# Performance work log

Measured on AMD Instinct MI355X. Metric: run time of the kernel, lower is better.

The kernel has to match this reference:

```python
import jax, jax.numpy as jnp
import numpy as np

E = 8            # num_experts
H = 1024         # hidden_size
I = 1024         # moe_intermediate_dim
T = 8192         # total tokens (sum of per-expert counts; no padding, grouped_mm path)
# Imbalanced routing, sums exactly to T
COUNTS = np.array([512, 1536, 1024, 768, 1280, 896, 1152, 1024], dtype=np.int32)


def setup_inputs() -> dict:
    key = jax.random.key(0)
    k_x, k_gu, k_d = jax.random.split(key, 3)
    x = jax.random.normal(k_x, (T, H), dtype=jnp.float32)
    # Weights stored pre-transposed: (E, H, 2I) and (E, I, H)
    gate_up_proj = jax.random.normal(k_gu, (E, H, 2 * I), dtype=jnp.float32) * (1.0 / np.sqrt(H))
    down_proj = jax.random.normal(k_d, (E, I, H), dtype=jnp.float32) * (1.0 / np.sqrt(I))
    num_tokens_per_expert = jnp.asarray(COUNTS)  # int32, sums to T
    return {
        "x": x,
        "gate_up_proj": gate_up_proj,
        "down_proj": down_proj,
        "num_tokens_per_expert": num_tokens_per_expert,
    }


def reference(x, gate_up_proj, down_proj, num_tokens_per_expert):
    # Grouped GEMM 1: [T,H] x [E,H,2I] with ragged group sizes -> [T,2I]
    gate_up = jax.lax.ragged_dot(x, gate_up_proj, group_sizes=num_tokens_per_expert)
    gate, up = jnp.split(gate_up, 2, axis=-1)
    h = jax.nn.silu(gate) * up  # SwiGLU: silu(gate) * up, [T,I]
    # Grouped GEMM 2: [T,I] x [E,I,H] -> [T,H]
    out = jax.lax.ragged_dot(h, down_proj, group_sizes=num_tokens_per_expert)
    return out.astype(x.dtype)
```

## Files before the change

### kernel.cpp

```cpp
#include <hip/hip_runtime.h>
#include <hip/hip_bf16.h>
#include <stdint.h>

#define E_ 8
#define H_ 1024
#define I_ 1024
#define T_ 8192
#define BM 128
#define BK 32
#define NKT 32

typedef __attribute__((ext_vector_type(4))) float f32x4;
typedef __attribute__((ext_vector_type(8))) short bf16x8;

__device__ __forceinline__ unsigned short f2bf(float f) {
  union { float f; unsigned int u; } v; v.f = f;
  unsigned int lsb = (v.u >> 16) & 1u;
  v.u += 0x7fffu + lsb;
  return (unsigned short)(v.u >> 16);
}

__device__ __forceinline__ void gload_lds16(const void* g, void* l) {
  __builtin_amdgcn_global_load_lds(
      (const __attribute__((address_space(1))) unsigned int*)g,
      (__attribute__((address_space(3))) unsigned int*)l,
      16, 0, 0);
}

__global__ void convert_f32_bf16(const float* __restrict__ in,
                                 unsigned short* __restrict__ out, int n) {
  int i = (blockIdx.x * blockDim.x + threadIdx.x) * 4;
  if (i >= n) return;
  float4 v = *reinterpret_cast<const float4*>(in + i);
  ushort4 o;
  o.x = f2bf(v.x); o.y = f2bf(v.y); o.z = f2bf(v.z); o.w = f2bf(v.w);
  *reinterpret_cast<ushort4*>(out + i) = o;
}

__global__ void transpose_f32_to_bf16(const float* __restrict__ in,
                                      unsigned short* __restrict__ out,
                                      int R, int C) {
  __shared__ float tile[64][33];
  int e = blockIdx.z;
  const float* inp = in + (size_t)e * R * C;
  unsigned short* outp = out + (size_t)e * R * C;
  int c0 = blockIdx.x * 32, r0 = blockIdx.y * 64;
  int tx = threadIdx.x, ty = threadIdx.y;
  for (int rr = ty; rr < 64; rr += 8)
    tile[rr][tx] = inp[(size_t)(r0 + rr) * C + c0 + tx];
  __syncthreads();
  for (int cc = ty; cc < 32; cc += 8) {
    ushort2 o;
    o.x = f2bf(tile[2 * tx][cc]);
    o.y = f2bf(tile[2 * tx + 1][cc]);
    *reinterpret_cast<ushort2*>(&outp[(size_t)(c0 + cc) * R + r0 + 2 * tx]) = o;
  }
}

__device__ __forceinline__ void find_tile(const int* counts, int ty,
                                          int& row_start, int& rows, int& expert) {
  int tacc = 0, off = 0;
  expert = 0; row_start = 0; rows = BM;
  #pragma unroll
  for (int e = 0; e < E_; ++e) {
    int c = counts[e];
    int te = (c + BM - 1) >> 7;
    if (ty >= tacc && ty < tacc + te) {
      expert = e;
      int lt = ty - tacc;
      row_start = off + lt * BM;
      rows = min(BM, c - lt * BM);
    }
    tacc += te; off += c;
  }
}

__launch_bounds__(256, 4)
__global__ void gemm1_swiglu(const unsigned short* __restrict__ X,
                             const unsigned short* __restrict__ W1T,
                             const int* __restrict__ counts,
                             unsigned short* __restrict__ Hout) {
  __shared__ unsigned short As[2][BM * BK];
  __shared__ unsigned short Bs[2][128 * BK];
  int id = blockIdx.x;
  int swz = (id & 7) * 128 + (id >> 3);
  int bn = swz & 15;
  int tyid = swz >> 4;
  int row_start, rows, expert;
  find_tile(counts, tyid, row_start, rows, expert);
  int tid = threadIdx.x, wid = tid >> 6, lane = tid & 63;
  int wr = wid >> 1, wc = wid & 1;
  const unsigned short* Wp = W1T + (size_t)expert * (2 * I_) * H_;

  f32x4 acc[4][4];
  #pragma unroll
  for (int m = 0; m < 4; ++m)
    #pragma unroll
    for (int n = 0; n < 4; ++n) acc[m][n] = {0.f, 0.f, 0.f, 0.f};

  int l4 = lane >> 2;
  int csw = ((lane & 3) ^ ((l4 >> 1) & 3)) * 8;
  int lr = lane & 15;
  int ck = ((lane >> 4) ^ ((lr >> 1) & 3)) * 8;

#define B1ROW(r) (((r) < 64) ? (bn * 64 + (r)) : (I_ + bn * 64 + ((r) - 64)))

#define STAGE1(buf, kt) do {                                                   \
    int k0 = (kt) * BK + csw;                                                  \
    _Pragma("unroll")                                                          \
    for (int i = 0; i < 2; ++i) {                                              \
      int r = wid * 32 + i * 16;                                               \
      int gr = row_start + min(r + l4, rows - 1);                              \
      gload_lds16(X + (size_t)gr * H_ + k0, &As[buf][r * BK]);                 \
    }                                                                          \
    _Pragma("unroll")                                                          \
    for (int i = 0; i < 2; ++i) {                                              \
      int r = wid * 32 + i * 16;                                               \
      int gn = B1ROW(r + l4);                                                  \
      gload_lds16(Wp + (size_t)gn * H_ + k0, &Bs[buf][r * BK]);                \
    }                                                                          \
  } while (0)

  STAGE1(0, 0);
  int cur = 0;
  for (int kt = 0; kt < NKT; ++kt) {
    STAGE1(cur ^ 1, min(kt + 1, NKT - 1));
    asm volatile("s_waitcnt vmcnt(4)" ::: "memory");
    __builtin_amdgcn_sched_barrier(0);
    __builtin_amdgcn_s_barrier();
    bf16x8 a[4], b[4];
    #pragma unroll
    for (int m = 0; m < 4; ++m)
      a[m] = *reinterpret_cast<const bf16x8*>(&As[cur][(wr * 64 + m * 16 + lr) * BK + ck]);
    #pragma unroll
    for (int n = 0; n < 2; ++n) {
      b[n]     = *reinterpret_cast<const bf16x8*>(&Bs[cur][(wc * 32 + n * 16 + lr) * BK + ck]);
      b[n + 2] = *reinterpret_cast<const bf16x8*>(&Bs[cur][(64 + wc * 32 + n * 16 + lr) * BK + ck]);
    }
    __builtin_amdgcn_s_setprio(1);
    #pragma unroll
    for (int m = 0; m < 4; ++m)
      #pragma unroll
      for (int n = 0; n < 4; ++n)
        acc[m][n] = __builtin_amdgcn_mfma_f32_16x16x32_bf16(a[m], b[n], acc[m][n], 0, 0, 0);
    __builtin_amdgcn_s_setprio(0);
    __builtin_amdgcn_sched_barrier(0);
    __builtin_amdgcn_s_barrier();
    cur ^= 1;
  }
#undef STAGE1
#undef B1ROW

  int lq = lane >> 4;
  #pragma unroll
  for (int m = 0; m < 4; ++m)
    #pragma unroll
    for (int n = 0; n < 2; ++n) {
      f32x4 g = acc[m][n], u = acc[m][n + 2];
      #pragma unroll
      for (int r = 0; r < 4; ++r) {
        int rl = wr * 64 + m * 16 + lq * 4 + r;
        if (rl < rows) {
          float gv = g[r];
          float hv = (gv / (1.f + __expf(-gv))) * u[r];
          Hout[(size_t)(row_start + rl) * I_ + bn * 64 + wc * 32 + n * 16 + lr] = f2bf(hv);
        }
      }
    }
}

__launch_bounds__(256, 4)
__global__ void gemm2(const unsigned short* __restrict__ Hin,
                      const unsigned short* __restrict__ W2T,
                      const int* __restrict__ counts,
                      float* __restrict__ Out) {
  __shared__ unsigned short As[2][BM * BK];
  __shared__ unsigned short Bs[2][64 * BK];
  int id = blockIdx.x;
  int swz = (id & 7) * 128 + (id >> 3);
  int bn = swz & 15;
  int tyid = swz >> 4;
  int row_start, rows, expert;
  find_tile(counts, tyid, row_start, rows, expert);
  int tid = threadIdx.x, wid = tid >> 6, lane = tid & 63;
  int wr = wid >> 1, wc = wid & 1;
  const unsigned short* Wp = W2T + (size_t)expert * H_ * I_;

  f32x4 acc[4][2];
  #pragma unroll
  for (int m = 0; m < 4; ++m)
    #pragma unroll
    for (int n = 0; n < 2; ++n) acc[m][n] = {0.f, 0.f, 0.f, 0.f};

  int l4 = lane >> 2;
  int csw = ((lane & 3) ^ ((l4 >> 1) & 3)) * 8;
  int lr = lane & 15;
  int ck = ((lane >> 4) ^ ((lr >> 1) & 3)) * 8;

#define STAGE2(buf, kt) do {                                                   \
    int k0 = (kt) * BK + csw;                                                  \
    _Pragma("unroll")                                                          \
    for (int i = 0; i < 2; ++i) {                                              \
      int r = wid * 32 + i * 16;                                               \
      int gr = row_start + min(r + l4, rows - 1);                              \
      gload_lds16(Hin + (size_t)gr * I_ + k0, &As[buf][r * BK]);               \
    }                                                                          \
    {                                                                          \
      int r = wid * 16;                                                        \
      int gn = bn * 64 + r + l4;                                               \
      gload_lds16(Wp + (size_t)gn * I_ + k0, &Bs[buf][r * BK]);                \
    }                                                                          \
  } while (0)

  STAGE2(0, 0);
  int cur = 0;
  for (int kt = 0; kt < NKT; ++kt) {
    STAGE2(cur ^ 1, min(kt + 1, NKT - 1));
    asm volatile("s_waitcnt vmcnt(3)" ::: "memory");
    __builtin_amdgcn_sched_barrier(0);
    __builtin_amdgcn_s_barrier();
    bf16x8 a[4], b[2];
    #pragma unroll
    for (int m = 0; m < 4; ++m)
      a[m] = *reinterpret_cast<const bf16x8*>(&As[cur][(wr * 64 + m * 16 + lr) * BK + ck]);
    #pragma unroll
    for (int n = 0; n < 2; ++n)
      b[n] = *reinterpret_cast<const bf16x8*>(&Bs[cur][(wc * 32 + n * 16 + lr) * BK + ck]);
    __builtin_amdgcn_s_setprio(1);
    #pragma unroll
    for (int m = 0; m < 4; ++m)
      #pragma unroll
      for (int n = 0; n < 2; ++n)
        acc[m][n] = __builtin_amdgcn_mfma_f32_16x16x32_bf16(a[m], b[n], acc[m][n], 0, 0, 0);
    __builtin_amdgcn_s_setprio(0);
    __builtin_amdgcn_sched_barrier(0);
    __builtin_amdgcn_s_barrier();
    cur ^= 1;
  }
#undef STAGE2

  int lq = lane >> 4;
  #pragma unroll
  for (int m = 0; m < 4; ++m)
    #pragma unroll
    for (int n = 0; n < 2; ++n)
      #pragma unroll
      for (int r = 0; r < 4; ++r) {
        int rl = wr * 64 + m * 16 + lq * 4 + r;
        if (rl < rows)
          Out[(size_t)(row_start + rl) * H_ + bn * 64 + wc * 32 + n * 16 + lr] =
              acc[m][n][r];
      }
}

extern "C" void kernel_launch(void* const* d_in, const int* in_sizes, int n_in,
                              void* d_out, int out_size, void* d_ws, size_t ws_size,
                              hipStream_t stream) {
  const float* x  = (const float*)d_in[0];
  const float* w1 = (const float*)d_in[1];
  const float* w2 = (const float*)d_in[2];
  const int* counts = (const int*)d_in[3];
  float* out = (float*)d_out;

  char* ws = (char*)d_ws;
  unsigned short* xb  = (unsigned short*)ws;
  unsigned short* w1t = (unsigned short*)(ws + (size_t)T_ * H_ * 2);
  unsigned short* w2t = (unsigned short*)(ws + (size_t)T_ * H_ * 2
                                             + (size_t)E_ * 2 * I_ * H_ * 2);
  unsigned short* hbuf = (unsigned short*)(ws + (size_t)T_ * H_ * 2
                                              + (size_t)E_ * 2 * I_ * H_ * 2
                                              + (size_t)E_ * H_ * I_ * 2);

  convert_f32_bf16<<<(T_ * H_) / 1024, 256, 0, stream>>>(x, xb, T_ * H_);
  dim3 tb(32, 8);
  transpose_f32_to_bf16<<<dim3((2 * I_) / 32, H_ / 64, E_), tb, 0, stream>>>(w1, w1t, H_, 2 * I_);
  transpose_f32_to_bf16<<<dim3(H_ / 32, I_ / 64, E_), tb, 0, stream>>>(w2, w2t, I_, H_);
  gemm1_swiglu<<<1024, 256, 0, stream>>>(xb, w1t, counts, hbuf);
  gemm2<<<1024, 256, 0, stream>>>(hbuf, w2t, counts, out);
}
```

Measured before the change: 118.1 us.

## Merge preprocessing launches, enlarge GEMM tiles, triple-buffer LDS pipeline

The three preprocessing kernels become two roles: x conversion and W1 transpose share one launch, and the W2 transpose moves into the gemm1 launch as extra blocks. Both GEMMs now use 128-wide N tiles, giving gemm1 a 128x256 tile over 4 waves, and switch from double to triple buffering with deeper prefetch. The aim is fewer launches, less redundant A-tile loading, and better hiding of memory latency. The cost is larger LDS and register use, which lowers occupancy (launch bounds 2 and 3), and the transpose blocks inside gemm1 compete with the GEMM blocks.

```diff
diff --git a/kernel.cpp b/kernel.cpp
--- a/kernel.cpp
+++ b/kernel.cpp
@@ -25,36 +25,6 @@
       (const __attribute__((address_space(1))) unsigned int*)g,
       (__attribute__((address_space(3))) unsigned int*)l,
       16, 0, 0);
-}
-
-__global__ void convert_f32_bf16(const float* __restrict__ in,
-                                 unsigned short* __restrict__ out, int n) {
-  int i = (blockIdx.x * blockDim.x + threadIdx.x) * 4;
-  if (i >= n) return;
-  float4 v = *reinterpret_cast<const float4*>(in + i);
-  ushort4 o;
-  o.x = f2bf(v.x); o.y = f2bf(v.y); o.z = f2bf(v.z); o.w = f2bf(v.w);
-  *reinterpret_cast<ushort4*>(out + i) = o;
-}
-
-__global__ void transpose_f32_to_bf16(const float* __restrict__ in,
-                                      unsigned short* __restrict__ out,
-                                      int R, int C) {
-  __shared__ float tile[64][33];
-  int e = blockIdx.z;
-  const float* inp = in + (size_t)e * R * C;
-  unsigned short* outp = out + (size_t)e * R * C;
-  int c0 = blockIdx.x * 32, r0 = blockIdx.y * 64;
-  int tx = threadIdx.x, ty = threadIdx.y;
-  for (int rr = ty; rr < 64; rr += 8)
-    tile[rr][tx] = inp[(size_t)(r0 + rr) * C + c0 + tx];
-  __syncthreads();
-  for (int cc = ty; cc < 32; cc += 8) {
-    ushort2 o;
-    o.x = f2bf(tile[2 * tx][cc]);
-    o.y = f2bf(tile[2 * tx + 1][cc]);
-    *reinterpret_cast<ushort2*>(&outp[(size_t)(c0 + cc) * R + r0 + 2 * tx]) = o;
-  }
 }
 
 __device__ __forceinline__ void find_tile(const int* counts, int ty,
@@ -75,26 +45,70 @@
   }
 }
 
-__launch_bounds__(256, 4)
-__global__ void gemm1_swiglu(const unsigned short* __restrict__ X,
-                             const unsigned short* __restrict__ W1T,
-                             const int* __restrict__ counts,
-                             unsigned short* __restrict__ Hout) {
-  __shared__ unsigned short As[2][BM * BK];
-  __shared__ unsigned short Bs[2][128 * BK];
+__device__ __forceinline__ void transpose_role(const float* inp,
+                                               unsigned short* outp,
+                                               int R, int C, int bx, int by,
+                                               void* smem) {
+  float (*tile)[33] = reinterpret_cast<float(*)[33]>(smem);
+  int c0 = bx * 32, r0 = by * 64;
+  int tx = threadIdx.x & 31, ty = threadIdx.x >> 5;
+  for (int rr = ty; rr < 64; rr += 8)
+    tile[rr][tx] = inp[(size_t)(r0 + rr) * C + c0 + tx];
+  __syncthreads();
+  for (int cc = ty; cc < 32; cc += 8) {
+    ushort2 o;
+    o.x = f2bf(tile[2 * tx][cc]);
+    o.y = f2bf(tile[2 * tx + 1][cc]);
+    *reinterpret_cast<ushort2*>(&outp[(size_t)(c0 + cc) * R + r0 + 2 * tx]) = o;
+  }
+}
+
+__global__ __launch_bounds__(256) void preproc_union(
+    const float* __restrict__ x, unsigned short* __restrict__ xb,
+    const float* __restrict__ w1, unsigned short* __restrict__ w1t) {
+  __shared__ float tile[64][33];
   int id = blockIdx.x;
-  int swz = (id & 7) * 128 + (id >> 3);
-  int bn = swz & 15;
-  int tyid = swz >> 4;
+  if (id < 8192) {
+    int i = (id * 256 + threadIdx.x) * 4;
+    float4 v = *reinterpret_cast<const float4*>(x + i);
+    ushort4 o;
+    o.x = f2bf(v.x); o.y = f2bf(v.y); o.z = f2bf(v.z); o.w = f2bf(v.w);
+    *reinterpret_cast<ushort4*>(xb + i) = o;
+    return;
+  }
+  int tb = id - 8192;
+  int bx = tb & 63, by = (tb >> 6) & 15, bz = tb >> 10;
+  transpose_role(w1 + (size_t)bz * H_ * 2 * I_,
+                 w1t + (size_t)bz * H_ * 2 * I_, H_, 2 * I_, bx, by, tile);
+}
+
+#define G1LDS (BM * BK + 256 * BK)
+__global__ __launch_bounds__(256, 2) void gemm1_union(
+    const unsigned short* __restrict__ X,
+    const unsigned short* __restrict__ W1T,
+    const int* __restrict__ counts,
+    unsigned short* __restrict__ Hout,
+    const float* __restrict__ w2, unsigned short* __restrict__ w2t) {
+  __shared__ unsigned short pool[3 * G1LDS];
+  if (blockIdx.x < 4096) {
+    int tb = blockIdx.x;
+    int bx = tb & 31, by = (tb >> 5) & 15, bz = tb >> 9;
+    transpose_role(w2 + (size_t)bz * I_ * H_,
+                   w2t + (size_t)bz * I_ * H_, I_, H_, bx, by, pool);
+    return;
+  }
+  int id = blockIdx.x - 4096;
+  int swz = (id & 7) * 64 + (id >> 3);
+  int bn = swz & 7;
+  int tyid = swz >> 3;
   int row_start, rows, expert;
   find_tile(counts, tyid, row_start, rows, expert);
   int tid = threadIdx.x, wid = tid >> 6, lane = tid & 63;
-  int wr = wid >> 1, wc = wid & 1;
   const unsigned short* Wp = W1T + (size_t)expert * (2 * I_) * H_;
 
-  f32x4 acc[4][4];
-  #pragma unroll
-  for (int m = 0; m < 4; ++m)
+  f32x4 acc[8][4];
+  #pragma unroll
+  for (int m = 0; m < 8; ++m)
     #pragma unroll
     for (int n = 0; n < 4; ++n) acc[m][n] = {0.f, 0.f, 0.f, 0.f};
 
@@ -103,94 +117,95 @@
   int lr = lane & 15;
   int ck = ((lane >> 4) ^ ((lr >> 1) & 3)) * 8;
 
-#define B1ROW(r) (((r) < 64) ? (bn * 64 + (r)) : (I_ + bn * 64 + ((r) - 64)))
-
 #define STAGE1(buf, kt) do {                                                   \
     int k0 = (kt) * BK + csw;                                                  \
+    unsigned short* Ab = pool + (buf) * G1LDS;                                 \
+    unsigned short* Bb = Ab + BM * BK;                                         \
     _Pragma("unroll")                                                          \
     for (int i = 0; i < 2; ++i) {                                              \
       int r = wid * 32 + i * 16;                                               \
       int gr = row_start + min(r + l4, rows - 1);                              \
-      gload_lds16(X + (size_t)gr * H_ + k0, &As[buf][r * BK]);                 \
-    }                                                                          \
-    _Pragma("unroll")                                                          \
-    for (int i = 0; i < 2; ++i) {                                              \
-      int r = wid * 32 + i * 16;                                               \
-      int gn = B1ROW(r + l4);                                                  \
-      gload_lds16(Wp + (size_t)gn * H_ + k0, &Bs[buf][r * BK]);                \
+      gload_lds16(X + (size_t)gr * H_ + k0, Ab + r * BK);                      \
+    }                                                                          \
+    _Pragma("unroll")                                                          \
+    for (int i = 0; i < 4; ++i) {                                              \
+      int r = wid * 64 + i * 16;                                               \
+      int rb = r + l4;                                                         \
+      int sub = rb & 63, ow = rb >> 6;                                         \
+      int col = (sub < 32) ? (bn * 128 + ow * 32 + sub)                        \
+                           : (I_ + bn * 128 + ow * 32 + sub - 32);             \
+      gload_lds16(Wp + (size_t)col * H_ + k0, Bb + r * BK);                    \
     }                                                                          \
   } while (0)
 
   STAGE1(0, 0);
-  int cur = 0;
+  STAGE1(1, 1);
   for (int kt = 0; kt < NKT; ++kt) {
-    STAGE1(cur ^ 1, min(kt + 1, NKT - 1));
-    asm volatile("s_waitcnt vmcnt(4)" ::: "memory");
-    __builtin_amdgcn_sched_barrier(0);
-    __builtin_amdgcn_s_barrier();
-    bf16x8 a[4], b[4];
-    #pragma unroll
-    for (int m = 0; m < 4; ++m)
-      a[m] = *reinterpret_cast<const bf16x8*>(&As[cur][(wr * 64 + m * 16 + lr) * BK + ck]);
-    #pragma unroll
-    for (int n = 0; n < 2; ++n) {
-      b[n]     = *reinterpret_cast<const bf16x8*>(&Bs[cur][(wc * 32 + n * 16 + lr) * BK + ck]);
-      b[n + 2] = *reinterpret_cast<const bf16x8*>(&Bs[cur][(64 + wc * 32 + n * 16 + lr) * BK + ck]);
-    }
+    STAGE1((kt + 2) % 3, min(kt + 2, NKT - 1));
+    asm volatile("s_waitcnt vmcnt(12)" ::: "memory");
+    __builtin_amdgcn_sched_barrier(0);
+    __builtin_amdgcn_s_barrier();
+    const unsigned short* Ab = pool + (kt % 3) * G1LDS;
+    const unsigned short* Bb = Ab + BM * BK;
+    bf16x8 a[8], b[4];
+    #pragma unroll
+    for (int m = 0; m < 8; ++m)
+      a[m] = *reinterpret_cast<const bf16x8*>(&Ab[(m * 16 + lr) * BK + ck]);
+    #pragma unroll
+    for (int n = 0; n < 4; ++n)
+      b[n] = *reinterpret_cast<const bf16x8*>(&Bb[(wid * 64 + n * 16 + lr) * BK + ck]);
     __builtin_amdgcn_s_setprio(1);
     #pragma unroll
-    for (int m = 0; m < 4; ++m)
+    for (int m = 0; m < 8; ++m)
       #pragma unroll
       for (int n = 0; n < 4; ++n)
         acc[m][n] = __builtin_amdgcn_mfma_f32_16x16x32_bf16(a[m], b[n], acc[m][n], 0, 0, 0);
     __builtin_amdgcn_s_setprio(0);
     __builtin_amdgcn_sched_barrier(0);
     __builtin_amdgcn_s_barrier();
-    cur ^= 1;
   }
 #undef STAGE1
-#undef B1ROW
 
   int lq = lane >> 4;
   #pragma unroll
-  for (int m = 0; m < 4; ++m)
+  for (int m = 0; m < 8; ++m)
     #pragma unroll
     for (int n = 0; n < 2; ++n) {
       f32x4 g = acc[m][n], u = acc[m][n + 2];
       #pragma unroll
       for (int r = 0; r < 4; ++r) {
-        int rl = wr * 64 + m * 16 + lq * 4 + r;
+        int rl = m * 16 + lq * 4 + r;
         if (rl < rows) {
           float gv = g[r];
           float hv = (gv / (1.f + __expf(-gv))) * u[r];
-          Hout[(size_t)(row_start + rl) * I_ + bn * 64 + wc * 32 + n * 16 + lr] = f2bf(hv);
+          Hout[(size_t)(row_start + rl) * I_ + bn * 128 + wid * 32 + n * 16 + lr] = f2bf(hv);
         }
       }
     }
 }
 
-__launch_bounds__(256, 4)
-__global__ void gemm2(const unsigned short* __restrict__ Hin,
-                      const unsigned short* __restrict__ W2T,
-                      const int* __restrict__ counts,
-                      float* __restrict__ Out) {
-  __shared__ unsigned short As[2][BM * BK];
-  __shared__ unsigned short Bs[2][64 * BK];
+#define G2LDS (BM * BK + BM * BK)
+__global__ __launch_bounds__(256, 3) void gemm2(
+    const unsigned short* __restrict__ Hin,
+    const unsigned short* __restrict__ W2T,
+    const int* __restrict__ counts,
+    float* __restrict__ Out) {
+  __shared__ unsigned short pool[3 * G2LDS];
   int id = blockIdx.x;
-  int swz = (id & 7) * 128 + (id >> 3);
-  int bn = swz & 15;
-  int tyid = swz >> 4;
+  int swz = (id & 7) * 64 + (id >> 3);
+  int bn = swz & 7;
+  int tyid = swz >> 3;
   int row_start, rows, expert;
   find_tile(counts, tyid, row_start, rows, expert);
   int tid = threadIdx.x, wid = tid >> 6, lane = tid & 63;
   int wr = wid >> 1, wc = wid & 1;
   const unsigned short* Wp = W2T + (size_t)expert * H_ * I_;
 
-  f32x4 acc[4][2];
+  f32x4 acc[4][4];
   #pragma unroll
   for (int m = 0; m < 4; ++m)
     #pragma unroll
-    for (int n = 0; n < 2; ++n) acc[m][n] = {0.f, 0.f, 0.f, 0.f};
+    for (int n = 0; n < 4; ++n) acc[m][n] = {0.f, 0.f, 0.f, 0.f};
 
   int l4 = lane >> 2;
   int csw = ((lane & 3) ^ ((l4 >> 1) & 3)) * 8;
@@ -199,43 +214,47 @@
 
 #define STAGE2(buf, kt) do {                                                   \
     int k0 = (kt) * BK + csw;                                                  \
+    unsigned short* Ab = pool + (buf) * G2LDS;                                 \
+    unsigned short* Bb = Ab + BM * BK;                                         \
     _Pragma("unroll")                                                          \
     for (int i = 0; i < 2; ++i) {                                              \
       int r = wid * 32 + i * 16;                                               \
       int gr = row_start + min(r + l4, rows - 1);                              \
-      gload_lds16(Hin + (size_t)gr * I_ + k0, &As[buf][r * BK]);               \
-    }                                                                          \
-    {                                                                          \
-      int r = wid * 16;                                                        \
-      int gn = bn * 64 + r + l4;                                               \
-      gload_lds16(Wp + (size_t)gn * I_ + k0, &Bs[buf][r * BK]);                \
+      gload_lds16(Hin + (size_t)gr * I_ + k0, Ab + r * BK);                    \
+    }                                                                          \
+    _Pragma("unroll")                                                          \
+    for (int i = 0; i < 2; ++i) {                                              \
+      int r = wid * 32 + i * 16;                                               \
+      int col = bn * 128 + r + l4;                                             \
+      gload_lds16(Wp + (size_t)col * I_ + k0, Bb + r * BK);                    \
     }                                                                          \
   } while (0)
 
   STAGE2(0, 0);
-  int cur = 0;
+  STAGE2(1, 1);
   for (int kt = 0; kt < NKT; ++kt) {
-    STAGE2(cur ^ 1, min(kt + 1, NKT - 1));
-    asm volatile("s_waitcnt vmcnt(3)" ::: "memory");
-    __builtin_amdgcn_sched_barrier(0);
-    __builtin_amdgcn_s_barrier();
-    bf16x8 a[4], b[2];
+    STAGE2((kt + 2) % 3, min(kt + 2, NKT - 1));
+    asm volatile("s_waitcnt vmcnt(8)" ::: "memory");
+    __builtin_amdgcn_sched_barrier(0);
+    __builtin_amdgcn_s_barrier();
+    const unsigned short* Ab = pool + (kt % 3) * G2LDS;
+    const unsigned short* Bb = Ab + BM * BK;
+    bf16x8 a[4], b[4];
     #pragma unroll
     for (int m = 0; m < 4; ++m)
-      a[m] = *reinterpret_cast<const bf16x8*>(&As[cur][(wr * 64 + m * 16 + lr) * BK + ck]);
-    #pragma unroll
-    for (int n = 0; n < 2; ++n)
-      b[n] = *reinterpret_cast<const bf16x8*>(&Bs[cur][(wc * 32 + n * 16 + lr) * BK + ck]);
+      a[m] = *reinterpret_cast<const bf16x8*>(&Ab[(wr * 64 + m * 16 + lr) * BK + ck]);
+    #pragma unroll
+    for (int n = 0; n < 4; ++n)
+      b[n] = *reinterpret_cast<const bf16x8*>(&Bb[(wc * 64 + n * 16 + lr) * BK + ck]);
     __builtin_amdgcn_s_setprio(1);
     #pragma unroll
     for (int m = 0; m < 4; ++m)
       #pragma unroll
-      for (int n = 0; n < 2; ++n)
+      for (int n = 0; n < 4; ++n)
         acc[m][n] = __builtin_amdgcn_mfma_f32_16x16x32_bf16(a[m], b[n], acc[m][n], 0, 0, 0);
     __builtin_amdgcn_s_setprio(0);
     __builtin_amdgcn_sched_barrier(0);
     __builtin_amdgcn_s_barrier();
-    cur ^= 1;
   }
 #undef STAGE2
 
@@ -243,12 +262,12 @@
   #pragma unroll
   for (int m = 0; m < 4; ++m)
     #pragma unroll
-    for (int n = 0; n < 2; ++n)
+    for (int n = 0; n < 4; ++n)
       #pragma unroll
       for (int r = 0; r < 4; ++r) {
         int rl = wr * 64 + m * 16 + lq * 4 + r;
         if (rl < rows)
-          Out[(size_t)(row_start + rl) * H_ + bn * 64 + wc * 32 + n * 16 + lr] =
+          Out[(size_t)(row_start + rl) * H_ + bn * 128 + wc * 64 + n * 16 + lr] =
               acc[m][n][r];
       }
 }
@@ -271,10 +290,7 @@
                                               + (size_t)E_ * 2 * I_ * H_ * 2
                                               + (size_t)E_ * H_ * I_ * 2);
 
-  convert_f32_bf16<<<(T_ * H_) / 1024, 256, 0, stream>>>(x, xb, T_ * H_);
-  dim3 tb(32, 8);
-  transpose_f32_to_bf16<<<dim3((2 * I_) / 32, H_ / 64, E_), tb, 0, stream>>>(w1, w1t, H_, 2 * I_);
-  transpose_f32_to_bf16<<<dim3(H_ / 32, I_ / 64, E_), tb, 0, stream>>>(w2, w2t, I_, H_);
-  gemm1_swiglu<<<1024, 256, 0, stream>>>(xb, w1t, counts, hbuf);
-  gemm2<<<1024, 256, 0, stream>>>(hbuf, w2t, counts, out);
-}
+  preproc_union<<<16384, 256, 0, stream>>>(x, xb, w1, w1t);
+  gemm1_union<<<4096 + 512, 256, 0, stream>>>(xb, w1t, counts, hbuf, w2, w2t);
+  gemm2<<<512, 256, 0, stream>>>(hbuf, w2t, counts, out);
+}
```

New measurement: 109.0 us. 7.7% less time.
